# Kernel optimization log

Hardware: AMD Instinct MI355X
Metric: run time of the kernel (lower is better)

Reference implementation:

```python
import jax, jax.numpy as jnp
import numpy as np

NEG_SLOPE = 0.2

def gatv2(x, edge_index, Wl, bl, Wr, br, att, bias):
    # PyG GATv2Conv (share_weights=False, add_self_loops=True, concat=True)
    N = x.shape[0]
    H, D = att.shape
    src0, dst0 = edge_index[0], edge_index[1]
    # remove_self_loops + add_self_loops semantics: mask existing self loops,
    # append one self loop per node (keeps static shapes under jit)
    loop = jnp.arange(N, dtype=src0.dtype)
    src = jnp.concatenate([src0, loop])
    dst = jnp.concatenate([dst0, loop])
    keep = jnp.concatenate([src0 != dst0, jnp.ones(N, dtype=bool)])  # drop original i->i edges
    xl = (x @ Wl + bl).reshape(N, H, D)  # source-side transform
    xr = (x @ Wr + br).reshape(N, H, D)  # target-side transform
    e = xl[src] + xr[dst]                                  # [E,H,D]
    logits = jnp.einsum('ehd,hd->eh', jax.nn.leaky_relu(e, NEG_SLOPE), att)
    logits = jnp.where(keep[:, None], logits, -jnp.inf)
    m = jax.ops.segment_max(logits, dst, num_segments=N)   # [N,H]
    ex = jnp.where(keep[:, None], jnp.exp(logits - m[dst]), 0.0)
    denom = jax.ops.segment_sum(ex, dst, num_segments=N)   # [N,H]
    alpha = ex / (denom[dst] + 1e-16)                      # [E,H]
    out = jax.ops.segment_sum(alpha[..., None] * xl[src], dst, num_segments=N)
    return out.reshape(N, H * D) + bias

def setup_inputs() -> dict:
    key = jax.random.key(0)
    ks = jax.random.split(key, 20)
    N, E, F, Hd = 50000, 400000, 5, 128
    s = 0.05
    inp = {
        'x': jax.random.normal(ks[0], (N, F), dtype=jnp.float32),
        'edge_index': jax.random.randint(ks[1], (2, E), 0, N, dtype=jnp.int64),
        # node_embed MLP
        'W1': jax.random.normal(ks[2], (F, Hd), dtype=jnp.float32) * s,
        'b1': jnp.zeros((Hd,), jnp.float32),
        'W2': jax.random.normal(ks[3], (Hd, Hd), dtype=jnp.float32) * s,
        'b2': jnp.zeros((Hd,), jnp.float32),
        # gnn1: GATv2Conv(128 -> 128, heads=4)
        'Wl1': jax.random.normal(ks[4], (Hd, 4 * Hd), dtype=jnp.float32) * s,
        'bl1': jnp.zeros((4 * Hd,), jnp.float32),
        'Wr1': jax.random.normal(ks[5], (Hd, 4 * Hd), dtype=jnp.float32) * s,
        'br1': jnp.zeros((4 * Hd,), jnp.float32),
        'att1': jax.random.normal(ks[6], (4, Hd), dtype=jnp.float32) * s,
        'bias1': jnp.zeros((4 * Hd,), jnp.float32),
        # gnn2: GATv2Conv(512 -> 128, heads=1)
        'Wl2': jax.random.normal(ks[7], (4 * Hd, Hd), dtype=jnp.float32) * s,
        'bl2': jnp.zeros((Hd,), jnp.float32),
        'Wr2': jax.random.normal(ks[8], (4 * Hd, Hd), dtype=jnp.float32) * s,
        'br2': jnp.zeros((Hd,), jnp.float32),
        'att2': jax.random.normal(ks[9], (1, Hd), dtype=jnp.float32) * s,
        'bias2': jnp.zeros((Hd,), jnp.float32),
    }
    return inp

def reference(x, edge_index, W1, b1, W2, b2, Wl1, bl1, Wr1, br1, att1, bias1,
              Wl2, bl2, Wr2, br2, att2, bias2):
    h = jax.nn.relu(x @ W1 + b1) @ W2 + b2                 # node_embed MLP
    h = jax.nn.relu(gatv2(h, edge_index, Wl1, bl1, Wr1, br1, att1, bias1))
    out = gatv2(h, edge_index, Wl2, bl2, Wr2, br2, att2, bias2)
    return out  # [N, 128]
```

## Files before the change

### kernel.cpp

```cpp
#include <hip/hip_runtime.h>
#include <math.h>

typedef __attribute__((ext_vector_type(8))) short bf16x8;
typedef __attribute__((ext_vector_type(4))) float f32x4;
typedef unsigned short ushort;
typedef unsigned int uint;

static __device__ __forceinline__ ushort f2bf(float f) {
    unsigned u = __float_as_uint(f);
    u = u + 0x7fff + ((u >> 16) & 1);
    return (ushort)(u >> 16);
}
static __device__ __forceinline__ float bf2f(ushort h) {
    return __uint_as_float(((unsigned)h) << 16);
}


__global__ void k_init(int* __restrict__ counts, int N) {
    int i = blockIdx.x * blockDim.x + threadIdx.x;
    if (i < N) counts[i] = 1;
}

__global__ void k_count(const int* __restrict__ src, const int* __restrict__ dst,
                        int E, int* __restrict__ counts) {
    int e = blockIdx.x * blockDim.x + threadIdx.x;
    if (e < E) {
        int s = src[e], d = dst[e];
        if (s != d) atomicAdd(&counts[d], 1);
    }
}

__global__ __launch_bounds__(256) void k_blocksum(const int* __restrict__ counts, int N,
                                                  int* __restrict__ bsum) {
    __shared__ int s[256];
    int t = threadIdx.x, i = blockIdx.x * 256 + t;
    s[t] = (i < N) ? counts[i] : 0;
    __syncthreads();
    for (int off = 128; off > 0; off >>= 1) {
        if (t < off) s[t] += s[t + off];
        __syncthreads();
    }
    if (t == 0) bsum[blockIdx.x] = s[0];
}

__global__ __launch_bounds__(256) void k_scanblocks(const int* __restrict__ bsum, int NB,
                                                    int* __restrict__ boff,
                                                    int* __restrict__ rowptr, int N) {
    __shared__ int s[256];
    int t = threadIdx.x;
    int v = (t < NB) ? bsum[t] : 0;
    s[t] = v;
    __syncthreads();
    for (int off = 1; off < 256; off <<= 1) {
        int u = (t >= off) ? s[t - off] : 0;
        __syncthreads();
        s[t] += u;
        __syncthreads();
    }
    if (t < NB) boff[t] = s[t] - v;
    if (t == NB - 1) rowptr[N] = s[t];
}

__global__ __launch_bounds__(256) void k_scatter(const int* __restrict__ counts, int N,
                                                 const int* __restrict__ boff,
                                                 int* __restrict__ rowptr,
                                                 int* __restrict__ cursor) {
    __shared__ int s[256];
    int t = threadIdx.x, i = blockIdx.x * 256 + t;
    int c = (i < N) ? counts[i] : 0;
    s[t] = c;
    __syncthreads();
    for (int off = 1; off < 256; off <<= 1) {
        int u = (t >= off) ? s[t - off] : 0;
        __syncthreads();
        s[t] += u;
        __syncthreads();
    }
    if (i < N) {
        int excl = boff[blockIdx.x] + s[t] - c;
        rowptr[i] = excl;
        cursor[i] = excl;
    }
}

__global__ void k_fill(const int* __restrict__ src, const int* __restrict__ dst,
                       int E, int N, int* __restrict__ cursor, int* __restrict__ colA) {
    int i = blockIdx.x * blockDim.x + threadIdx.x;
    if (i < E) {
        int s = src[i], d = dst[i];
        if (s != d) { int p = atomicAdd(&cursor[d], 1); colA[p] = s; }
    } else if (i < E + N) {
        int n = i - E;
        int p = atomicAdd(&cursor[n], 1); colA[p] = n;
    }
}


__global__ __launch_bounds__(256) void k_repack(
    const float* __restrict__ W2, const float* __restrict__ Wl1,
    const float* __restrict__ Wr1, const float* __restrict__ Wl2,
    const float* __restrict__ Wr2,
    ushort* __restrict__ wfh, ushort* __restrict__ wfl)
{
    int job = blockIdx.y;
    int t = blockIdx.x * 256 + threadIdx.x;
    int ks = t >> 9, n = (t >> 6) & 7, l = t & 63;

    const float* W; int ldw, rowoff, col0;
    if (job == 0)      { W = W2;  ldw = 128; rowoff = 0;              col0 = 0; }
    else if (job < 5)  { W = Wl1; ldw = 512; rowoff = 0;              col0 = (job - 1) * 128; }
    else if (job < 9)  { W = Wr1; ldw = 512; rowoff = 0;              col0 = (job - 5) * 128; }
    else if (job < 13) { W = Wl2; ldw = 128; rowoff = (job - 9) * 128;  col0 = 0; }
    else               { W = Wr2; ldw = 128; rowoff = (job - 13) * 128; col0 = 0; }

    int krow = rowoff + ks * 32 + (l >> 4) * 8;
    int col = col0 + n * 16 + (l & 15);
    size_t dbase = (size_t)job * 16384 + (((size_t)(ks * 8 + n)) * 64 + l) * 8;
#pragma unroll
    for (int j = 0; j < 8; j++) {
        float v = W[(size_t)(krow + j) * ldw + col];
        ushort h = f2bf(v);
        ushort lo = f2bf(v - bf2f(h));
        wfh[dbase + j] = h;
        wfl[dbase + j] = lo;
    }
}


__global__ __launch_bounds__(256) void k_mlp1(
    const float* __restrict__ x, const float* __restrict__ W1, const float* __restrict__ b1,
    ushort* __restrict__ out, int N)
{
    int n = blockIdx.x * 2 + (threadIdx.x >> 7);
    int j = threadIdx.x & 127;
    if (n >= N) return;
    float s = b1[j];
#pragma unroll
    for (int k = 0; k < 5; k++) s = fmaf(x[(size_t)n * 5 + k], W1[k * 128 + j], s);
    s = fmaxf(s, 0.f);
    out[(size_t)n * 128 + j] = f2bf(s);
}


__global__ __launch_bounds__(256) void gemm_h0(
    const ushort* __restrict__ A,
    const ushort* __restrict__ wfh, const ushort* __restrict__ wfl,
    const float* __restrict__ bias,
    ushort* __restrict__ C, int M)
{
    int tid = threadIdx.x;
    int w = tid >> 6, l = tid & 63;
    int m0 = blockIdx.x * 128 + w * 32;
    int lr = l & 15, kg = l >> 4;

    f32x4 acc[2][8];
#pragma unroll
    for (int i = 0; i < 2; i++)
#pragma unroll
        for (int j = 0; j < 8; j++) acc[i][j] = (f32x4){0.f, 0.f, 0.f, 0.f};

    int row0 = m0 + lr, row1 = m0 + 16 + lr;
    bool ok0 = row0 < M, ok1 = row1 < M;
    const bf16x8 zz = {0, 0, 0, 0, 0, 0, 0, 0};

#pragma unroll
    for (int ks = 0; ks < 4; ks++) {
        int koff = ks * 32 + kg * 8;
        bf16x8 a0 = ok0 ? *(const bf16x8*)(A + (size_t)row0 * 128 + koff) : zz;
        bf16x8 a1 = ok1 ? *(const bf16x8*)(A + (size_t)row1 * 128 + koff) : zz;
#pragma unroll
        for (int n = 0; n < 8; n++) {
            size_t bo = (((size_t)(ks * 8 + n)) * 64 + l) * 8;
            bf16x8 bh = *(const bf16x8*)(wfh + bo);
            bf16x8 bl = *(const bf16x8*)(wfl + bo);
            acc[0][n] = __builtin_amdgcn_mfma_f32_16x16x32_bf16(a0, bh, acc[0][n], 0, 0, 0);
            acc[0][n] = __builtin_amdgcn_mfma_f32_16x16x32_bf16(a0, bl, acc[0][n], 0, 0, 0);
            acc[1][n] = __builtin_amdgcn_mfma_f32_16x16x32_bf16(a1, bh, acc[1][n], 0, 0, 0);
            acc[1][n] = __builtin_amdgcn_mfma_f32_16x16x32_bf16(a1, bl, acc[1][n], 0, 0, 0);
        }
    }

#pragma unroll
    for (int mf = 0; mf < 2; mf++) {
#pragma unroll
        for (int r = 0; r < 4; r++) {
            int row = m0 + mf * 16 + kg * 4 + r;
            if (row >= M) continue;
#pragma unroll
            for (int n = 0; n < 8; n++) {
                size_t idx = (size_t)row * 128 + n * 16 + lr;
                C[idx] = f2bf(acc[mf][n][r] + bias[n * 16 + lr]);
            }
        }
    }
}


__global__ __launch_bounds__(256) void gemm_xlr1(
    const ushort* __restrict__ A,
    const ushort* __restrict__ wh, const ushort* __restrict__ wl,
    const float* __restrict__ bl1, const float* __restrict__ br1,
    ushort* __restrict__ out, int M)
{
    __shared__ __align__(16) ushort Bh[16384];
    __shared__ __align__(16) ushort Bl[16384];

    int tid = threadIdx.x;
    int w = tid >> 6, l = tid & 63;
    int m0 = blockIdx.x * 128 + w * 32;
    int lr = l & 15, kg = l >> 4;

    int row0 = m0 + lr, row1 = m0 + 16 + lr;
    bool ok0 = row0 < M, ok1 = row1 < M;
    const bf16x8 zz = {0, 0, 0, 0, 0, 0, 0, 0};

    bf16x8 a0[4], a1[4];
#pragma unroll
    for (int ks = 0; ks < 4; ks++) {
        int koff = ks * 32 + kg * 8;
        a0[ks] = ok0 ? *(const bf16x8*)(A + (size_t)row0 * 128 + koff) : zz;
        a1[ks] = ok1 ? *(const bf16x8*)(A + (size_t)row1 * 128 + koff) : zz;
    }

    for (int t = 0; t < 8; t++) {
        __syncthreads();
        {
            const float4* gh = (const float4*)(wh + (size_t)t * 16384);
            const float4* gl = (const float4*)(wl + (size_t)t * 16384);
            float4* sh = (float4*)Bh;
            float4* sl = (float4*)Bl;
#pragma unroll
            for (int i = 0; i < 8; i++) {
                sh[i * 256 + tid] = gh[i * 256 + tid];
                sl[i * 256 + tid] = gl[i * 256 + tid];
            }
        }
        __syncthreads();

        f32x4 acc[2][8];
#pragma unroll
        for (int i = 0; i < 2; i++)
#pragma unroll
            for (int j = 0; j < 8; j++) acc[i][j] = (f32x4){0.f, 0.f, 0.f, 0.f};

#pragma unroll
        for (int ks = 0; ks < 4; ks++) {
#pragma unroll
            for (int n = 0; n < 8; n++) {
                int bo = ((ks * 8 + n) * 64 + l) * 8;
                bf16x8 bh = *(const bf16x8*)(Bh + bo);
                bf16x8 bl = *(const bf16x8*)(Bl + bo);
                acc[0][n] = __builtin_amdgcn_mfma_f32_16x16x32_bf16(a0[ks], bh, acc[0][n], 0, 0, 0);
                acc[0][n] = __builtin_amdgcn_mfma_f32_16x16x32_bf16(a0[ks], bl, acc[0][n], 0, 0, 0);
                acc[1][n] = __builtin_amdgcn_mfma_f32_16x16x32_bf16(a1[ks], bh, acc[1][n], 0, 0, 0);
                acc[1][n] = __builtin_amdgcn_mfma_f32_16x16x32_bf16(a1[ks], bl, acc[1][n], 0, 0, 0);
            }
        }

        float bcol[8];
#pragma unroll
        for (int n = 0; n < 8; n++)
            bcol[n] = (t < 4) ? bl1[t * 128 + n * 16 + lr] : br1[(t - 4) * 128 + n * 16 + lr];

#pragma unroll
        for (int mf = 0; mf < 2; mf++) {
#pragma unroll
            for (int r = 0; r < 4; r++) {
                int row = m0 + mf * 16 + kg * 4 + r;
                if (row >= M) continue;
#pragma unroll
                for (int n = 0; n < 8; n++)
                    out[(size_t)row * 1024 + t * 128 + n * 16 + lr] = f2bf(acc[mf][n][r] + bcol[n]);
            }
        }
    }
}


__global__ __launch_bounds__(256) void gemm_xlr2(
    const ushort* __restrict__ A,
    const ushort* __restrict__ wfh, const ushort* __restrict__ wfl,
    const float* __restrict__ bl2, const float* __restrict__ br2,
    ushort* __restrict__ xl2, ushort* __restrict__ xr2, int M)
{
    __shared__ __align__(16) ushort Bh[16384];
    __shared__ __align__(16) ushort Bl[16384];

    int tid = threadIdx.x;
    int w = tid >> 6, l = tid & 63;
    int m0 = blockIdx.x * 64 + w * 16;
    int lr = l & 15, kg = l >> 4;

    int row0 = m0 + lr;
    bool ok0 = row0 < M;
    const bf16x8 zz = {0, 0, 0, 0, 0, 0, 0, 0};

    f32x4 acc[2][8];
#pragma unroll
    for (int i = 0; i < 2; i++)
#pragma unroll
        for (int j = 0; j < 8; j++) acc[i][j] = (f32x4){0.f, 0.f, 0.f, 0.f};

    for (int kc = 0; kc < 4; kc++) {
        bf16x8 ah[4];
#pragma unroll
        for (int ks = 0; ks < 4; ks++)
            ah[ks] = ok0 ? *(const bf16x8*)(A + (size_t)row0 * 512 + kc * 128 + ks * 32 + kg * 8) : zz;

        for (int t = 0; t < 2; t++) {
            int slot = 9 + t * 4 + kc;
            __syncthreads();
            {
                const float4* gh = (const float4*)(wfh + (size_t)slot * 16384);
                const float4* gl = (const float4*)(wfl + (size_t)slot * 16384);
                float4* sh = (float4*)Bh;
                float4* sl = (float4*)Bl;
#pragma unroll
                for (int i = 0; i < 8; i++) {
                    sh[i * 256 + tid] = gh[i * 256 + tid];
                    sl[i * 256 + tid] = gl[i * 256 + tid];
                }
            }
            __syncthreads();
#pragma unroll
            for (int ks = 0; ks < 4; ks++) {
#pragma unroll
                for (int n = 0; n < 8; n++) {
                    int bo = ((ks * 8 + n) * 64 + l) * 8;
                    bf16x8 bh = *(const bf16x8*)(Bh + bo);
                    bf16x8 bl = *(const bf16x8*)(Bl + bo);
                    acc[t][n] = __builtin_amdgcn_mfma_f32_16x16x32_bf16(ah[ks], bh, acc[t][n], 0, 0, 0);
                    acc[t][n] = __builtin_amdgcn_mfma_f32_16x16x32_bf16(ah[ks], bl, acc[t][n], 0, 0, 0);
                }
            }
        }
    }

#pragma unroll
    for (int r = 0; r < 4; r++) {
        int row = m0 + kg * 4 + r;
        if (row >= M) continue;
#pragma unroll
        for (int n = 0; n < 8; n++) {
            int col = n * 16 + lr;
            xl2[(size_t)row * 128 + col] = f2bf(acc[0][n][r] + bl2[col]);
            xr2[(size_t)row * 128 + col] = f2bf(acc[1][n][r] + br2[col]);
        }
    }
}


__global__ __launch_bounds__(256) void gat_edge4(
    const ushort* __restrict__ xlr,
    const float* __restrict__ att,
    const float* __restrict__ bias,
    const int* __restrict__ rowptr, const int* __restrict__ colA,
    ushort* __restrict__ h1,
    int N)
{
    int n = blockIdx.x;
    int h = threadIdx.x >> 6, l = threadIdx.x & 63;
    int g = l >> 4, q = l & 15;

    const ushort* xlbase = xlr + h * 128 + q * 8;

    bf16x8 xrv = *(const bf16x8*)(xlr + (size_t)n * 1024 + (4 + h) * 128 + q * 8);
    float4 ata = *(const float4*)(att + h * 128 + q * 8);
    float4 atb = *(const float4*)(att + h * 128 + q * 8 + 4);
    float xr[8] , at[8] = {ata.x, ata.y, ata.z, ata.w, atb.x, atb.y, atb.z, atb.w};
#pragma unroll
    for (int j = 0; j < 8; j++) xr[j] = bf2f((ushort)xrv[j]);

    auto dotc = [&](bf16x8 v8, float* vv) -> float {
        float c = 0.f;
#pragma unroll
        for (int j = 0; j < 8; j++) {
            vv[j] = bf2f((ushort)v8[j]);
            float t = vv[j] + xr[j];
            t = (t > 0.f) ? t : 0.2f * t;
            c = fmaf(t, at[j], c);
        }
        c += __shfl_xor(c, 1);
        c += __shfl_xor(c, 2);
        c += __shfl_xor(c, 4);
        c += __shfl_xor(c, 8);
        return c;
    };

    float tmp[8];
    bf16x8 vself = *(const bf16x8*)(xlbase + (size_t)n * 1024);
    float cs = dotc(vself, tmp);

    int k0 = rowptr[n], k1 = rowptr[n + 1];
    float s = 0.f, o[8];
#pragma unroll
    for (int j = 0; j < 8; j++) o[j] = 0.f;

    auto edge = [&](bf16x8 v8) {
        float vv[8];
        float c = dotc(v8, vv);
        float p = __expf(fminf(c - cs, 80.f));
        s += p;
#pragma unroll
        for (int j = 0; j < 8; j++) o[j] = fmaf(p, vv[j], o[j]);
    };

    for (int base = k0 + g; base < k1; base += 16) {
        int x0 = colA[base];
        int x1 = (base + 4  < k1) ? colA[base + 4]  : -1;
        int x2 = (base + 8  < k1) ? colA[base + 8]  : -1;
        int x3 = (base + 12 < k1) ? colA[base + 12] : -1;
        int y1 = (x1 >= 0) ? x1 : n;
        int y2 = (x2 >= 0) ? x2 : n;
        int y3 = (x3 >= 0) ? x3 : n;
        bf16x8 v0 = *(const bf16x8*)(xlbase + (size_t)x0 * 1024);
        bf16x8 v1 = *(const bf16x8*)(xlbase + (size_t)y1 * 1024);
        bf16x8 v2 = *(const bf16x8*)(xlbase + (size_t)y2 * 1024);
        bf16x8 v3 = *(const bf16x8*)(xlbase + (size_t)y3 * 1024);
        edge(v0);
        if (x1 >= 0) edge(v1);
        if (x2 >= 0) edge(v2);
        if (x3 >= 0) edge(v3);
    }

#pragma unroll
    for (int off = 16; off <= 32; off <<= 1) {
        s += __shfl_xor(s, off);
#pragma unroll
        for (int j = 0; j < 8; j++) o[j] += __shfl_xor(o[j], off);
    }

    if (g == 0) {
        float inv = 1.f / (s + 1e-16f);
        float4 ba = *(const float4*)(bias + h * 128 + q * 8);
        float4 bb = *(const float4*)(bias + h * 128 + q * 8 + 4);
        float bs[8] = {ba.x, ba.y, ba.z, ba.w, bb.x, bb.y, bb.z, bb.w};
        bf16x8 pk;
#pragma unroll
        for (int j = 0; j < 8; j++)
            pk[j] = (short)f2bf(fmaxf(o[j] * inv + bs[j], 0.f));
        *(bf16x8*)(h1 + (size_t)n * 512 + h * 128 + q * 8) = pk;
    }
}


__global__ __launch_bounds__(256) void gat_edge1(
    const ushort* __restrict__ xl, const ushort* __restrict__ xr,
    const float* __restrict__ att, const float* __restrict__ bias,
    const int* __restrict__ rowptr, const int* __restrict__ colA,
    float* __restrict__ out, int N)
{
    int n = blockIdx.x * 4 + (threadIdx.x >> 6);
    if (n >= N) return;
    int l = threadIdx.x & 63;
    int g = l >> 4, q = l & 15;

    const ushort* xlbase = xl + q * 8;

    bf16x8 xrv = *(const bf16x8*)(xr + (size_t)n * 128 + q * 8);
    float4 ata = *(const float4*)(att + q * 8);
    float4 atb = *(const float4*)(att + q * 8 + 4);
    float xrr[8], at[8] = {ata.x, ata.y, ata.z, ata.w, atb.x, atb.y, atb.z, atb.w};
#pragma unroll
    for (int j = 0; j < 8; j++) xrr[j] = bf2f((ushort)xrv[j]);

    auto dotc = [&](bf16x8 v8, float* vv) -> float {
        float c = 0.f;
#pragma unroll
        for (int j = 0; j < 8; j++) {
            vv[j] = bf2f((ushort)v8[j]);
            float t = vv[j] + xrr[j];
            t = (t > 0.f) ? t : 0.2f * t;
            c = fmaf(t, at[j], c);
        }
        c += __shfl_xor(c, 1);
        c += __shfl_xor(c, 2);
        c += __shfl_xor(c, 4);
        c += __shfl_xor(c, 8);
        return c;
    };

    float tmp[8];
    bf16x8 vself = *(const bf16x8*)(xlbase + (size_t)n * 128);
    float cs = dotc(vself, tmp);

    int k0 = rowptr[n], k1 = rowptr[n + 1];
    float s = 0.f, o[8];
#pragma unroll
    for (int j = 0; j < 8; j++) o[j] = 0.f;

    auto edge = [&](bf16x8 v8) {
        float vv[8];
        float c = dotc(v8, vv);
        float p = __expf(fminf(c - cs, 80.f));
        s += p;
#pragma unroll
        for (int j = 0; j < 8; j++) o[j] = fmaf(p, vv[j], o[j]);
    };

    for (int base = k0 + g; base < k1; base += 16) {
        int x0 = colA[base];
        int x1 = (base + 4  < k1) ? colA[base + 4]  : -1;
        int x2 = (base + 8  < k1) ? colA[base + 8]  : -1;
        int x3 = (base + 12 < k1) ? colA[base + 12] : -1;
        int y1 = (x1 >= 0) ? x1 : n;
        int y2 = (x2 >= 0) ? x2 : n;
        int y3 = (x3 >= 0) ? x3 : n;
        bf16x8 v0 = *(const bf16x8*)(xlbase + (size_t)x0 * 128);
        bf16x8 v1 = *(const bf16x8*)(xlbase + (size_t)y1 * 128);
        bf16x8 v2 = *(const bf16x8*)(xlbase + (size_t)y2 * 128);
        bf16x8 v3 = *(const bf16x8*)(xlbase + (size_t)y3 * 128);
        edge(v0);
        if (x1 >= 0) edge(v1);
        if (x2 >= 0) edge(v2);
        if (x3 >= 0) edge(v3);
    }

#pragma unroll
    for (int off = 16; off <= 32; off <<= 1) {
        s += __shfl_xor(s, off);
#pragma unroll
        for (int j = 0; j < 8; j++) o[j] += __shfl_xor(o[j], off);
    }

    if (g == 0) {
        float inv = 1.f / (s + 1e-16f);
        float4 ba = *(const float4*)(bias + q * 8);
        float4 bb = *(const float4*)(bias + q * 8 + 4);
        float4 r0, r1;
        r0.x = o[0] * inv + ba.x;  r0.y = o[1] * inv + ba.y;
        r0.z = o[2] * inv + ba.z;  r0.w = o[3] * inv + ba.w;
        r1.x = o[4] * inv + bb.x;  r1.y = o[5] * inv + bb.y;
        r1.z = o[6] * inv + bb.z;  r1.w = o[7] * inv + bb.w;
        *(float4*)(out + (size_t)n * 128 + q * 8)     = r0;
        *(float4*)(out + (size_t)n * 128 + q * 8 + 4) = r1;
    }
}


extern "C" void kernel_launch(void* const* d_in, const int* in_sizes, int n_in,
                              void* d_out, int out_size, void* d_ws, size_t ws_size,
                              hipStream_t stream) {
    const float* x    = (const float*)d_in[0];
    const int* ei     = (const int*)d_in[1];
    const float* W1   = (const float*)d_in[2];
    const float* b1   = (const float*)d_in[3];
    const float* W2   = (const float*)d_in[4];
    const float* b2   = (const float*)d_in[5];
    const float* Wl1  = (const float*)d_in[6];
    const float* bl1  = (const float*)d_in[7];
    const float* Wr1  = (const float*)d_in[8];
    const float* br1  = (const float*)d_in[9];
    const float* att1 = (const float*)d_in[10];
    const float* bias1= (const float*)d_in[11];
    const float* Wl2  = (const float*)d_in[12];
    const float* bl2  = (const float*)d_in[13];
    const float* Wr2  = (const float*)d_in[14];
    const float* br2  = (const float*)d_in[15];
    const float* att2 = (const float*)d_in[16];
    const float* bias2= (const float*)d_in[17];

    int E = in_sizes[1] / 2;
    int N = in_sizes[0] / 5;
    const int* srcE = ei;
    const int* dstE = ei + E;

    float* dout = (float*)d_out;

    ushort* xlr1 = (ushort*)d_ws;
    ushort* h1   = xlr1 + (size_t)N * 1024;
    ushort* h0   = h1 + (size_t)N * 512;
    ushort* xr2  = h0 + (size_t)N * 128;
    ushort* wfh  = xr2 + (size_t)N * 128;
    ushort* wfl  = wfh + 17 * 16384;
    int* rowptr = (int*)(wfl + 17 * 16384);
    int* cursor = rowptr + (N + 1);
    int* counts = cursor + N;
    int* colA   = counts + N;
    int* bsum   = colA + (E + N);
    int* boff   = bsum + 256;

    ushort* cC  = h1;
    ushort* xl2 = h0;

    int NB = (N + 255) / 256;

    k_init <<<(N + 255) / 256, 256, 0, stream>>>(counts, N);
    k_count<<<(E + 255) / 256, 256, 0, stream>>>(srcE, dstE, E, counts);
    k_blocksum <<<NB, 256, 0, stream>>>(counts, N, bsum);
    k_scanblocks<<<1, 256, 0, stream>>>(bsum, NB, boff, rowptr, N);
    k_scatter  <<<NB, 256, 0, stream>>>(counts, N, boff, rowptr, cursor);
    k_fill <<<(E + N + 255) / 256, 256, 0, stream>>>(srcE, dstE, E, N, cursor, colA);

    {
        dim3 g(8, 17);
        k_repack<<<g, 256, 0, stream>>>(W2, Wl1, Wr1, Wl2, Wr2, wfh, wfl);
    }

    int mb128 = (N + 127) / 128;
    int mb64  = (N + 63) / 64;

    k_mlp1<<<(N + 1) / 2, 256, 0, stream>>>(x, W1, b1, cC, N);
    gemm_h0<<<mb128, 256, 0, stream>>>(cC, wfh, wfl, b2, h0, N);

    gemm_xlr1<<<mb128, 256, 0, stream>>>(h0, wfh + 16384, wfl + 16384,
                                         bl1, br1, xlr1, N);
    gat_edge4<<<N, 256, 0, stream>>>(xlr1, att1, bias1, rowptr, colA, h1, N);

    gemm_xlr2<<<mb64, 256, 0, stream>>>(h1, wfh, wfl, bl2, br2, xl2, xr2, N);
    gat_edge1<<<(N + 3) / 4, 256, 0, stream>>>(xl2, xr2, att2, bias2, rowptr, colA, dout, N);
}
```

Baseline: 380.0 us.

## Split xl/xr GEMMs over output-tile grid dimension, read weights directly from global

```diff
diff --git a/kernel.cpp b/kernel.cpp
--- a/kernel.cpp
+++ b/kernel.cpp
@@ -15,11 +15,6 @@
     return __uint_as_float(((unsigned)h) << 16);
 }
 
-
-__global__ void k_init(int* __restrict__ counts, int N) {
-    int i = blockIdx.x * blockDim.x + threadIdx.x;
-    if (i < N) counts[i] = 1;
-}
 
 __global__ void k_count(const int* __restrict__ src, const int* __restrict__ dst,
                         int E, int* __restrict__ counts) {
@@ -58,7 +53,7 @@
         __syncthreads();
     }
     if (t < NB) boff[t] = s[t] - v;
-    if (t == NB - 1) rowptr[N] = s[t];
+    if (t == NB - 1) rowptr[N] = s[t] + N;
 }
 
 __global__ __launch_bounds__(256) void k_scatter(const int* __restrict__ counts, int N,
@@ -77,7 +72,7 @@
         __syncthreads();
     }
     if (i < N) {
-        int excl = boff[blockIdx.x] + s[t] - c;
+        int excl = boff[blockIdx.x] + s[t] - c + i;
         rowptr[i] = excl;
         cursor[i] = excl;
     }
@@ -202,149 +197,122 @@
     const float* __restrict__ bl1, const float* __restrict__ br1,
     ushort* __restrict__ out, int M)
 {
-    __shared__ __align__(16) ushort Bh[16384];
-    __shared__ __align__(16) ushort Bl[16384];
-
+    int t = blockIdx.y;
     int tid = threadIdx.x;
     int w = tid >> 6, l = tid & 63;
     int m0 = blockIdx.x * 128 + w * 32;
     int lr = l & 15, kg = l >> 4;
 
+    const ushort* bh_base = wh + (size_t)t * 16384;
+    const ushort* bl_base = wl + (size_t)t * 16384;
+
+    f32x4 acc[2][8];
+#pragma unroll
+    for (int i = 0; i < 2; i++)
+#pragma unroll
+        for (int j = 0; j < 8; j++) acc[i][j] = (f32x4){0.f, 0.f, 0.f, 0.f};
+
     int row0 = m0 + lr, row1 = m0 + 16 + lr;
     bool ok0 = row0 < M, ok1 = row1 < M;
     const bf16x8 zz = {0, 0, 0, 0, 0, 0, 0, 0};
 
-    bf16x8 a0[4], a1[4];
 #pragma unroll
     for (int ks = 0; ks < 4; ks++) {
         int koff = ks * 32 + kg * 8;
-        a0[ks] = ok0 ? *(const bf16x8*)(A + (size_t)row0 * 128 + koff) : zz;
-        a1[ks] = ok1 ? *(const bf16x8*)(A + (size_t)row1 * 128 + koff) : zz;
-    }
-
-    for (int t = 0; t < 8; t++) {
-        __syncthreads();
-        {
-            const float4* gh = (const float4*)(wh + (size_t)t * 16384);
-            const float4* gl = (const float4*)(wl + (size_t)t * 16384);
-            float4* sh = (float4*)Bh;
-            float4* sl = (float4*)Bl;
-#pragma unroll
-            for (int i = 0; i < 8; i++) {
-                sh[i * 256 + tid] = gh[i * 256 + tid];
-                sl[i * 256 + tid] = gl[i * 256 + tid];
-            }
-        }
-        __syncthreads();
-
-        f32x4 acc[2][8];
-#pragma unroll
-        for (int i = 0; i < 2; i++)
-#pragma unroll
-            for (int j = 0; j < 8; j++) acc[i][j] = (f32x4){0.f, 0.f, 0.f, 0.f};
-
+        bf16x8 a0 = ok0 ? *(const bf16x8*)(A + (size_t)row0 * 128 + koff) : zz;
+        bf16x8 a1 = ok1 ? *(const bf16x8*)(A + (size_t)row1 * 128 + koff) : zz;
+#pragma unroll
+        for (int n = 0; n < 8; n++) {
+            size_t bo = (((size_t)(ks * 8 + n)) * 64 + l) * 8;
+            bf16x8 bh = *(const bf16x8*)(bh_base + bo);
+            bf16x8 bl = *(const bf16x8*)(bl_base + bo);
+            acc[0][n] = __builtin_amdgcn_mfma_f32_16x16x32_bf16(a0, bh, acc[0][n], 0, 0, 0);
+            acc[0][n] = __builtin_amdgcn_mfma_f32_16x16x32_bf16(a0, bl, acc[0][n], 0, 0, 0);
+            acc[1][n] = __builtin_amdgcn_mfma_f32_16x16x32_bf16(a1, bh, acc[1][n], 0, 0, 0);
+            acc[1][n] = __builtin_amdgcn_mfma_f32_16x16x32_bf16(a1, bl, acc[1][n], 0, 0, 0);
+        }
+    }
+
+    float bcol[8];
+#pragma unroll
+    for (int n = 0; n < 8; n++)
+        bcol[n] = (t < 4) ? bl1[t * 128 + n * 16 + lr] : br1[(t - 4) * 128 + n * 16 + lr];
+
+#pragma unroll
+    for (int mf = 0; mf < 2; mf++) {
+#pragma unroll
+        for (int r = 0; r < 4; r++) {
+            int row = m0 + mf * 16 + kg * 4 + r;
+            if (row >= M) continue;
+#pragma unroll
+            for (int n = 0; n < 8; n++)
+                out[(size_t)row * 1024 + t * 128 + n * 16 + lr] = f2bf(acc[mf][n][r] + bcol[n]);
+        }
+    }
+}
+
+
+__global__ __launch_bounds__(256) void gemm_xlr2(
+    const ushort* __restrict__ A,
+    const ushort* __restrict__ wfh, const ushort* __restrict__ wfl,
+    const float* __restrict__ bl2, const float* __restrict__ br2,
+    ushort* __restrict__ xl2, ushort* __restrict__ xr2, int M)
+{
+    int t = blockIdx.y;
+    int tid = threadIdx.x;
+    int w = tid >> 6, l = tid & 63;
+    int m0 = blockIdx.x * 128 + w * 32;
+    int lr = l & 15, kg = l >> 4;
+
+    f32x4 acc[2][8];
+#pragma unroll
+    for (int i = 0; i < 2; i++)
+#pragma unroll
+        for (int j = 0; j < 8; j++) acc[i][j] = (f32x4){0.f, 0.f, 0.f, 0.f};
+
+    int row0 = m0 + lr, row1 = m0 + 16 + lr;
+    bool ok0 = row0 < M, ok1 = row1 < M;
+    const bf16x8 zz = {0, 0, 0, 0, 0, 0, 0, 0};
+
+    for (int kc = 0; kc < 4; kc++) {
+        const ushort* bh_base = wfh + (size_t)(9 + t * 4 + kc) * 16384;
+        const ushort* bl_base = wfl + (size_t)(9 + t * 4 + kc) * 16384;
+        bf16x8 a0[4], a1[4];
 #pragma unroll
         for (int ks = 0; ks < 4; ks++) {
+            int koff = kc * 128 + ks * 32 + kg * 8;
+            a0[ks] = ok0 ? *(const bf16x8*)(A + (size_t)row0 * 512 + koff) : zz;
+            a1[ks] = ok1 ? *(const bf16x8*)(A + (size_t)row1 * 512 + koff) : zz;
+        }
+#pragma unroll
+        for (int ks = 0; ks < 4; ks++) {
 #pragma unroll
             for (int n = 0; n < 8; n++) {
-                int bo = ((ks * 8 + n) * 64 + l) * 8;
-                bf16x8 bh = *(const bf16x8*)(Bh + bo);
-                bf16x8 bl = *(const bf16x8*)(Bl + bo);
+                size_t bo = (((size_t)(ks * 8 + n)) * 64 + l) * 8;
+                bf16x8 bh = *(const bf16x8*)(bh_base + bo);
+                bf16x8 bl = *(const bf16x8*)(bl_base + bo);
                 acc[0][n] = __builtin_amdgcn_mfma_f32_16x16x32_bf16(a0[ks], bh, acc[0][n], 0, 0, 0);
                 acc[0][n] = __builtin_amdgcn_mfma_f32_16x16x32_bf16(a0[ks], bl, acc[0][n], 0, 0, 0);
                 acc[1][n] = __builtin_amdgcn_mfma_f32_16x16x32_bf16(a1[ks], bh, acc[1][n], 0, 0, 0);
                 acc[1][n] = __builtin_amdgcn_mfma_f32_16x16x32_bf16(a1[ks], bl, acc[1][n], 0, 0, 0);
             }
         }
-
-        float bcol[8];
-#pragma unroll
-        for (int n = 0; n < 8; n++)
-            bcol[n] = (t < 4) ? bl1[t * 128 + n * 16 + lr] : br1[(t - 4) * 128 + n * 16 + lr];
-
-#pragma unroll
-        for (int mf = 0; mf < 2; mf++) {
-#pragma unroll
-            for (int r = 0; r < 4; r++) {
-                int row = m0 + mf * 16 + kg * 4 + r;
-                if (row >= M) continue;
-#pragma unroll
-                for (int n = 0; n < 8; n++)
-                    out[(size_t)row * 1024 + t * 128 + n * 16 + lr] = f2bf(acc[mf][n][r] + bcol[n]);
+    }
+
+    const float* bias = (t == 0) ? bl2 : br2;
+    ushort* outp = (t == 0) ? xl2 : xr2;
+
+#pragma unroll
+    for (int mf = 0; mf < 2; mf++) {
+#pragma unroll
+        for (int r = 0; r < 4; r++) {
+            int row = m0 + mf * 16 + kg * 4 + r;
+            if (row >= M) continue;
+#pragma unroll
+            for (int n = 0; n < 8; n++) {
+                int col = n * 16 + lr;
+                outp[(size_t)row * 128 + col] = f2bf(acc[mf][n][r] + bias[col]);
             }
-        }
-    }
-}
-
-
-__global__ __launch_bounds__(256) void gemm_xlr2(
-    const ushort* __restrict__ A,
-    const ushort* __restrict__ wfh, const ushort* __restrict__ wfl,
-    const float* __restrict__ bl2, const float* __restrict__ br2,
-    ushort* __restrict__ xl2, ushort* __restrict__ xr2, int M)
-{
-    __shared__ __align__(16) ushort Bh[16384];
-    __shared__ __align__(16) ushort Bl[16384];
-
-    int tid = threadIdx.x;
-    int w = tid >> 6, l = tid & 63;
-    int m0 = blockIdx.x * 64 + w * 16;
-    int lr = l & 15, kg = l >> 4;
-
-    int row0 = m0 + lr;
-    bool ok0 = row0 < M;
-    const bf16x8 zz = {0, 0, 0, 0, 0, 0, 0, 0};
-
-    f32x4 acc[2][8];
-#pragma unroll
-    for (int i = 0; i < 2; i++)
-#pragma unroll
-        for (int j = 0; j < 8; j++) acc[i][j] = (f32x4){0.f, 0.f, 0.f, 0.f};
-
-    for (int kc = 0; kc < 4; kc++) {
-        bf16x8 ah[4];
-#pragma unroll
-        for (int ks = 0; ks < 4; ks++)
-            ah[ks] = ok0 ? *(const bf16x8*)(A + (size_t)row0 * 512 + kc * 128 + ks * 32 + kg * 8) : zz;
-
-        for (int t = 0; t < 2; t++) {
-            int slot = 9 + t * 4 + kc;
-            __syncthreads();
-            {
-                const float4* gh = (const float4*)(wfh + (size_t)slot * 16384);
-                const float4* gl = (const float4*)(wfl + (size_t)slot * 16384);
-                float4* sh = (float4*)Bh;
-                float4* sl = (float4*)Bl;
-#pragma unroll
-                for (int i = 0; i < 8; i++) {
-                    sh[i * 256 + tid] = gh[i * 256 + tid];
-                    sl[i * 256 + tid] = gl[i * 256 + tid];
-                }
-            }
-            __syncthreads();
-#pragma unroll
-            for (int ks = 0; ks < 4; ks++) {
-#pragma unroll
-                for (int n = 0; n < 8; n++) {
-                    int bo = ((ks * 8 + n) * 64 + l) * 8;
-                    bf16x8 bh = *(const bf16x8*)(Bh + bo);
-                    bf16x8 bl = *(const bf16x8*)(Bl + bo);
-                    acc[t][n] = __builtin_amdgcn_mfma_f32_16x16x32_bf16(ah[ks], bh, acc[t][n], 0, 0, 0);
-                    acc[t][n] = __builtin_amdgcn_mfma_f32_16x16x32_bf16(ah[ks], bl, acc[t][n], 0, 0, 0);
-                }
-            }
-        }
-    }
-
-#pragma unroll
-    for (int r = 0; r < 4; r++) {
-        int row = m0 + kg * 4 + r;
-        if (row >= M) continue;
-#pragma unroll
-        for (int n = 0; n < 8; n++) {
-            int col = n * 16 + lr;
-            xl2[(size_t)row * 128 + col] = f2bf(acc[0][n][r] + bl2[col]);
-            xr2[(size_t)row * 128 + col] = f2bf(acc[1][n][r] + br2[col]);
         }
     }
 }
@@ -585,7 +553,7 @@
 
     int NB = (N + 255) / 256;
 
-    k_init <<<(N + 255) / 256, 256, 0, stream>>>(counts, N);
+    hipMemsetAsync(counts, 0, (size_t)N * sizeof(int), stream);
     k_count<<<(E + 255) / 256, 256, 0, stream>>>(srcE, dstE, E, counts);
     k_blocksum <<<NB, 256, 0, stream>>>(counts, N, bsum);
     k_scanblocks<<<1, 256, 0, stream>>>(bsum, NB, boff, rowptr, N);
@@ -598,15 +566,19 @@
     }
 
     int mb128 = (N + 127) / 128;
-    int mb64  = (N + 63) / 64;
 
     k_mlp1<<<(N + 1) / 2, 256, 0, stream>>>(x, W1, b1, cC, N);
     gemm_h0<<<mb128, 256, 0, stream>>>(cC, wfh, wfl, b2, h0, N);
 
-    gemm_xlr1<<<mb128, 256, 0, stream>>>(h0, wfh + 16384, wfl + 16384,
-                                         bl1, br1, xlr1, N);
+    {
+        dim3 g(mb128, 8);
+        gemm_xlr1<<<g, 256, 0, stream>>>(h0, wfh + 16384, wfl + 16384, bl1, br1, xlr1, N);
+    }
     gat_edge4<<<N, 256, 0, stream>>>(xlr1, att1, bias1, rowptr, colA, h1, N);
 
-    gemm_xlr2<<<mb64, 256, 0, stream>>>(h1, wfh, wfl, bl2, br2, xl2, xr2, N);
+    {
+        dim3 g(mb128, 2);
+        gemm_xlr2<<<g, 256, 0, stream>>>(h1, wfh, wfl, bl2, br2, xl2, xr2, N);
+    }
     gat_edge1<<<(N + 3) / 4, 256, 0, stream>>>(xl2, xr2, att2, bias2, rowptr, colA, dout, N);
 }
```

New measurement: 406.1 us. +6.9%, slower.
